# Performance work log

Measured on AMD Instinct MI355X. Metric: run time of the kernel, lower is better.

## Reference

```python
import jax, jax.numpy as jnp
import numpy as np

N, F, K, FP = 4096, 256, 8, 64  # nodes, in-feat, heads, out-feat per head
NEG_SLOPE = 0.2
MASK_FILL = -1e30  # stand-in for -inf (numerically safe under softmax/vjp)


def setup_inputs() -> dict:
    key = jax.random.key(0)
    k1, k2, k3, k4, k5 = jax.random.split(key, 5)
    x = jax.random.normal(k1, (N, F), dtype=jnp.float32)
    mask = jax.random.randint(k2, (1, N, N), 0, 2).astype(bool)
    idx = jnp.arange(N)
    mask = mask.at[0, idx, idx].set(True)  # self-loops guarantee no empty softmax rows
    W_w = jax.random.normal(k3, (K * FP, F), dtype=jnp.float32) * (1.0 / np.sqrt(F))
    W_b = jnp.zeros((K * FP,), dtype=jnp.float32)
    a_left = jax.random.normal(k4, (1, K, FP), dtype=jnp.float32) * 0.1
    a_right = jax.random.normal(k5, (1, K, FP), dtype=jnp.float32) * 0.1
    return {"x": x, "W_w": W_w, "W_b": W_b, "a_left": a_left, "a_right": a_right, "mask": mask}


def reference(x, W_w, W_b, a_left, a_right, mask):
    k, fp = a_left.shape[1], a_left.shape[2]
    # W(x): (N, K*F') -> (N, K, F')   [dropout p=0.0 -> identity]
    xe = (x @ W_w.T + W_b).reshape(-1, k, fp)
    # additive scores: h_left (K,N,1) + h_right (K,1,N) -> e (K,N,N)
    hl = jnp.einsum('nkf,kf->kn', xe, a_left[0])
    hr = jnp.einsum('nkf,kf->kn', xe, a_right[0])
    e = hl[:, :, None] + hr[:, None, :]
    e = jnp.where(e > 0, e, NEG_SLOPE * e)          # LeakyReLU(0.2)
    e = jnp.where(mask, e, MASK_FILL)               # masked_fill(~mask, -inf)
    a = jax.nn.softmax(e, axis=-1)                  # (K,N,N)
    # weighted sum of neighbor features: (K,N,N) x (N,K,F') -> (N,K,F')
    h_prime = jnp.einsum('knm,mkf->nkf', a, xe)
    h_prime = jax.nn.elu(h_prime)
    # non-final layer: elu again (as in source) then concat heads
    out = jax.nn.elu(h_prime).reshape(-1, k * fp)   # (N, K*F')
    return (out, mask)
```

## Files before the change

### kernel.cpp

```cpp
#include <hip/hip_runtime.h>
#include <hip/hip_bf16.h>

#define N_NODES 4096
#define F_IN    256
#define KH      8
#define KF      512
#define NEG_SLOPE 0.2f
#define EBIAS   4.0f

typedef _Float16 half8v __attribute__((ext_vector_type(8)));
typedef _Float16 half2v __attribute__((ext_vector_type(2)));
typedef __attribute__((ext_vector_type(4))) float floatx4;

union H8U4 { half8v v; unsigned u[4]; };

__device__ __forceinline__ unsigned short f2h(float f) {
    _Float16 h = (_Float16)f;
    unsigned short u; __builtin_memcpy(&u, &h, 2);
    return u;
}
__device__ __forceinline__ half2v asH2(unsigned u) {
    half2v h; __builtin_memcpy(&h, &u, 4);
    return h;
}
__device__ __forceinline__ unsigned asU(half2v h) {
    unsigned u; __builtin_memcpy(&u, &h, 4);
    return u;
}

__global__ __launch_bounds__(256) void mask_fused(
    const int* __restrict__ mask, float* __restrict__ outm,
    unsigned long long* __restrict__ bits) {
  const int tid = threadIdx.x;
  const size_t t4 = (size_t)blockIdx.x * 256 + tid;
  const int4 mv = ((const int4*)mask)[t4];
  float4 o;
  o.x = mv.x ? 1.f : 0.f; o.y = mv.y ? 1.f : 0.f;
  o.z = mv.z ? 1.f : 0.f; o.w = mv.w ? 1.f : 0.f;
  ((float4*)outm)[t4] = o;
  const unsigned nib = (mv.x ? 1u : 0u) | (mv.y ? 2u : 0u) |
                       (mv.z ? 4u : 0u) | (mv.w ? 8u : 0u);
  unsigned long long wv = (unsigned long long)nib << (4 * (tid & 15));
  wv |= __shfl_xor(wv, 1);
  wv |= __shfl_xor(wv, 2);
  wv |= __shfl_xor(wv, 4);
  wv |= __shfl_xor(wv, 8);
  if ((tid & 15) == 0) {
    const size_t e0 = t4 << 2;
    const size_t n = e0 >> 12;
    const size_t c = (e0 & 4095) >> 6;
    bits[c * N_NODES + n] = wv;
  }
}

__global__ __launch_bounds__(256) void mask_pack(
    const int* __restrict__ mask, unsigned long long* __restrict__ bits) {
  const size_t idx = (size_t)blockIdx.x * 256 + threadIdx.x;
  const unsigned long long b = __ballot(mask[idx] != 0);
  if ((threadIdx.x & 63) == 0) {
    const size_t w = idx >> 6;
    bits[(w & 63) * (size_t)N_NODES + (w >> 6)] = b;
  }
}
__global__ __launch_bounds__(256) void mask_copy(
    const int* __restrict__ mask, float* __restrict__ outm) {
  const size_t i4 = (size_t)blockIdx.x * 256 + threadIdx.x;
  const int4 mv = ((const int4*)mask)[i4];
  float4 o;
  o.x = mv.x ? 1.f : 0.f; o.y = mv.y ? 1.f : 0.f;
  o.z = mv.z ? 1.f : 0.f; o.w = mv.w ? 1.f : 0.f;
  ((float4*)outm)[i4] = o;
}

__global__ __launch_bounds__(256) void xe_gemm(
    const float* __restrict__ x,
    const float* __restrict__ Ww,
    const float* __restrict__ Wb,
    const float* __restrict__ al,
    const float* __restrict__ ar,
    unsigned short* __restrict__ xeB,
    float* __restrict__ hl,
    unsigned* __restrict__ EA,
    unsigned* __restrict__ EB,
    float* __restrict__ bmax) {
  __shared__ float As[32][65];
  __shared__ float Bs[32][65];
  __shared__ float redmax[4];
  const int tid = threadIdx.x;
  const int n0 = blockIdx.x * 64;
  const int j0 = blockIdx.y * 64;
  const int lr = tid >> 2;
  const int lc = (tid & 3) * 8;
  const int ty = tid >> 4;
  const int tx = tid & 15;
  float c[4][4];
  #pragma unroll
  for (int i = 0; i < 4; ++i)
    #pragma unroll
    for (int j = 0; j < 4; ++j) c[i][j] = 0.f;

  for (int f0 = 0; f0 < F_IN; f0 += 32) {
    const float* ap = x  + (size_t)(n0 + lr) * F_IN + f0 + lc;
    const float* bp = Ww + (size_t)(j0 + lr) * F_IN + f0 + lc;
    const float4 a0 = *(const float4*)ap;
    const float4 a1 = *(const float4*)(ap + 4);
    const float4 b0 = *(const float4*)bp;
    const float4 b1 = *(const float4*)(bp + 4);
    __syncthreads();
    As[lc + 0][lr] = a0.x; As[lc + 1][lr] = a0.y;
    As[lc + 2][lr] = a0.z; As[lc + 3][lr] = a0.w;
    As[lc + 4][lr] = a1.x; As[lc + 5][lr] = a1.y;
    As[lc + 6][lr] = a1.z; As[lc + 7][lr] = a1.w;
    Bs[lc + 0][lr] = b0.x; Bs[lc + 1][lr] = b0.y;
    Bs[lc + 2][lr] = b0.z; Bs[lc + 3][lr] = b0.w;
    Bs[lc + 4][lr] = b1.x; Bs[lc + 5][lr] = b1.y;
    Bs[lc + 6][lr] = b1.z; Bs[lc + 7][lr] = b1.w;
    __syncthreads();
    #pragma unroll
    for (int kk = 0; kk < 32; ++kk) {
      const float4 av = *(const float4*)&As[kk][ty * 4];
      const float4 bv = *(const float4*)&Bs[kk][tx * 4];
      const float a4[4] = {av.x, av.y, av.z, av.w};
      const float b4[4] = {bv.x, bv.y, bv.z, bv.w};
      #pragma unroll
      for (int i = 0; i < 4; ++i)
        #pragma unroll
        for (int j = 0; j < 4; ++j) c[i][j] = fmaf(a4[i], b4[j], c[i][j]);
    }
  }
  const float4 wb4 = *(const float4*)(Wb + j0 + tx * 4);
  const float4 al4 = *(const float4*)(al + j0 + tx * 4);
  const float4 ar4 = *(const float4*)(ar + j0 + tx * 4);
  const float wb[4] = {wb4.x, wb4.y, wb4.z, wb4.w};
  const float alv[4] = {al4.x, al4.y, al4.z, al4.w};
  const float arv[4] = {ar4.x, ar4.y, ar4.z, ar4.w};
  float v[4][4];
  float pl[4], pr[4];
  #pragma unroll
  for (int i = 0; i < 4; ++i) {
    float sl = 0.f, sr = 0.f;
    #pragma unroll
    for (int j = 0; j < 4; ++j) {
      v[i][j] = c[i][j] + wb[j];
      sl = fmaf(v[i][j], alv[j], sl);
      sr = fmaf(v[i][j], arv[j], sr);
    }
    pl[i] = sl; pr[i] = sr;
  }
  {
    const int k   = blockIdx.y;
    const int ft  = tx >> 2;
    const int fb  = (tx & 3) * 4;
    const int cc  = blockIdx.x;
    const int h_  = ty >> 3;
    const int qd  = (ty >> 1) & 3;
    const int jj0 = (ty & 1) * 4;
    unsigned short* tile = xeB + ((((size_t)(k * 4 + ft)) * 64 + cc) << 10)
                         + h_ * 512 + qd * 8 + jj0;
    #pragma unroll
    for (int j = 0; j < 4; ++j) {
      ushort4 pk;
      pk.x = f2h(v[0][j]); pk.y = f2h(v[1][j]);
      pk.z = f2h(v[2][j]); pk.w = f2h(v[3][j]);
      *(ushort4*)(tile + (fb + j) * 32) = pk;
    }
  }
  #pragma unroll
  for (int off = 8; off > 0; off >>= 1) {
    #pragma unroll
    for (int i = 0; i < 4; ++i) {
      pl[i] += __shfl_down(pl[i], off);
      pr[i] += __shfl_down(pr[i], off);
    }
  }
  if (tx == 0) {
    const int k = blockIdx.y;
    float4 o0 = {pl[0], pl[1], pl[2], pl[3]};
    *(float4*)(hl + k * N_NODES + n0 + ty * 4) = o0;
    unsigned short e1[4], e2[4];
    #pragma unroll
    for (int i = 0; i < 4; ++i) {
      e1[i] = f2h(__expf(pr[i] - EBIAS));
      e2[i] = f2h(__expf(NEG_SLOPE * (pr[i] - EBIAS)));
    }
    uint2 wa, wbv;
    wa.x  = (unsigned)e1[0] | ((unsigned)e1[1] << 16);
    wa.y  = (unsigned)e1[2] | ((unsigned)e1[3] << 16);
    wbv.x = (unsigned)e2[0] | ((unsigned)e2[1] << 16);
    wbv.y = (unsigned)e2[2] | ((unsigned)e2[3] << 16);
    *(uint2*)(EA + k * 2048 + ((n0 + ty * 4) >> 1)) = wa;
    *(uint2*)(EB + k * 2048 + ((n0 + ty * 4) >> 1)) = wbv;
  }
  float bm = (tx == 0)
      ? fmaxf(fmaxf(pr[0], pr[1]), fmaxf(pr[2], pr[3])) : -1e30f;
  bm = fmaxf(bm, __shfl_xor(bm, 16));
  bm = fmaxf(bm, __shfl_xor(bm, 32));
  if ((tid & 63) == 0) redmax[tid >> 6] = bm;
  __syncthreads();
  if (tid == 0) {
    bmax[blockIdx.y * 64 + blockIdx.x] =
        fmaxf(fmaxf(redmax[0], redmax[1]), fmaxf(redmax[2], redmax[3]));
  }
}

__global__ __launch_bounds__(256, 2) void gat_attn(
    const unsigned long long* __restrict__ mbitsT,
    const float* __restrict__ hl,
    const float* __restrict__ bmax,
    const unsigned* __restrict__ EA,
    const unsigned* __restrict__ EB,
    const unsigned short* __restrict__ xeB,
    float* __restrict__ out) {
  __shared__ float lds_acc[4][64][20];
  const int t = threadIdx.x;
  const int w4 = t >> 6;
  const int lane = t & 63;
  const int k  = blockIdx.x & 7;
  const int rg = blockIdx.x >> 3;
  const int n0 = rg * 32;
  const int row = lane & 15;
  const int quad = lane >> 4;
  const int q8 = quad * 8;

  float hm = bmax[k * 64 + lane];
  #pragma unroll
  for (int o = 1; o < 64; o <<= 1) hm = fmaxf(hm, __shfl_xor(hm, o));

  const float* hlp = hl + k * N_NODES + n0 + row;
  const float hlA = hlp[0];
  const float hlB = hlp[16];
  const float sA = hlA + hm;
  const float MA = fmaxf(sA, NEG_SLOPE * sA);
  const float sB = hlB + hm;
  const float MB = fmaxf(sB, NEG_SLOPE * sB);
  const float c1Af = __expf(hlA + EBIAS - MA);
  const float c2Af = __expf(NEG_SLOPE * (hlA + EBIAS) - MA);
  const float c1Bf = __expf(hlB + EBIAS - MB);
  const float c2Bf = __expf(NEG_SLOPE * (hlB + EBIAS) - MB);
  const half2v c1A = {(_Float16)c1Af, (_Float16)c1Af};
  const half2v c2A = {(_Float16)c2Af, (_Float16)c2Af};
  const half2v c1B = {(_Float16)c1Bf, (_Float16)c1Bf};
  const half2v c2B = {(_Float16)c2Bf, (_Float16)c2Bf};

  const int c0 = w4 * 16;
  const int cEnd = c0 + 16;

  const unsigned* pEA = EA + k * 2048 + c0 * 32 + quad * 4;
  const unsigned* pEB = EB + k * 2048 + c0 * 32 + quad * 4;
  const unsigned long long* pM = mbitsT + (size_t)c0 * N_NODES + n0 + row;
  const unsigned short* pB = xeB + (((size_t)k * 4) << 16)
                           + ((size_t)c0 << 10) + row * 32 + q8;

  half8v ones;
  #pragma unroll
  for (int i = 0; i < 8; ++i) ones[i] = (_Float16)1.0f;

  floatx4 accA[4], accB[4];
  #pragma unroll
  for (int ft = 0; ft < 4; ++ft) {
    accA[ft] = (floatx4){0.f, 0.f, 0.f, 0.f};
    accB[ft] = (floatx4){0.f, 0.f, 0.f, 0.f};
  }
  floatx4 dpA = (floatx4){0.f, 0.f, 0.f, 0.f};
  floatx4 dpB = (floatx4){0.f, 0.f, 0.f, 0.f};

  uint4 pA0 = *(const uint4*)pEA;
  uint4 pA1 = *(const uint4*)(pEA + 16);
  uint4 pB0 = *(const uint4*)pEB;
  uint4 pB1 = *(const uint4*)(pEB + 16);
  unsigned long long pMvA = pM[0];
  unsigned long long pMvB = pM[16];

  for (int cc = c0; cc < cEnd; ++cc) {
    half8v b0, b1, b2, b3, b4, b5, b6, b7;
    b0 = *(const half8v*)pB;                     b1 = *(const half8v*)(pB + 512);
    b2 = *(const half8v*)(pB + (64 << 10));      b3 = *(const half8v*)(pB + (64 << 10) + 512);
    b4 = *(const half8v*)(pB + (128 << 10));     b5 = *(const half8v*)(pB + (128 << 10) + 512);
    b6 = *(const half8v*)(pB + (192 << 10));     b7 = *(const half8v*)(pB + (192 << 10) + 512);
    pB += 1024;
    const uint4 eA0 = pA0, eA1 = pA1, eB0 = pB0, eB1 = pB1;
    const unsigned long long mbA = pMvA, mbB = pMvB;
    pEA += 32; pEB += 32; pM += N_NODES;
    if (cc + 1 < cEnd) {
      pA0 = *(const uint4*)pEA;
      pA1 = *(const uint4*)(pEA + 16);
      pB0 = *(const uint4*)pEB;
      pB1 = *(const uint4*)(pEB + 16);
      pMvA = pM[0];
      pMvB = pM[16];
    }
    const unsigned ea_lo[4] = {eA0.x, eA0.y, eA0.z, eA0.w};
    const unsigned eb_lo[4] = {eB0.x, eB0.y, eB0.z, eB0.w};
    const unsigned ea_hi[4] = {eA1.x, eA1.y, eA1.z, eA1.w};
    const unsigned eb_hi[4] = {eB1.x, eB1.y, eB1.z, eB1.w};
    {
      const unsigned mlo = (unsigned)(mbA >> q8);
      const unsigned mhi = (unsigned)(mbA >> (32 + q8));
      H8U4 a0, a1;
      #pragma unroll
      for (int p = 0; p < 4; ++p) {
        const half2v w2 = __builtin_elementwise_max(c1A * asH2(ea_lo[p]),
                                                    c2A * asH2(eb_lo[p]));
        const unsigned tb = mlo >> (2 * p);
        a0.u[p] = asU(w2) & (((tb & 1u) | ((tb & 2u) << 15)) * 0xFFFFu);
      }
      #pragma unroll
      for (int p = 0; p < 4; ++p) {
        const half2v w2 = __builtin_elementwise_max(c1A * asH2(ea_hi[p]),
                                                    c2A * asH2(eb_hi[p]));
        const unsigned tb = mhi >> (2 * p);
        a1.u[p] = asU(w2) & (((tb & 1u) | ((tb & 2u) << 15)) * 0xFFFFu);
      }
      dpA = __builtin_amdgcn_mfma_f32_16x16x32_f16(a0.v, ones, dpA, 0, 0, 0);
      dpA = __builtin_amdgcn_mfma_f32_16x16x32_f16(a1.v, ones, dpA, 0, 0, 0);
      accA[0] = __builtin_amdgcn_mfma_f32_16x16x32_f16(a0.v, b0, accA[0], 0, 0, 0);
      accA[0] = __builtin_amdgcn_mfma_f32_16x16x32_f16(a1.v, b1, accA[0], 0, 0, 0);
      accA[1] = __builtin_amdgcn_mfma_f32_16x16x32_f16(a0.v, b2, accA[1], 0, 0, 0);
      accA[1] = __builtin_amdgcn_mfma_f32_16x16x32_f16(a1.v, b3, accA[1], 0, 0, 0);
      accA[2] = __builtin_amdgcn_mfma_f32_16x16x32_f16(a0.v, b4, accA[2], 0, 0, 0);
      accA[2] = __builtin_amdgcn_mfma_f32_16x16x32_f16(a1.v, b5, accA[2], 0, 0, 0);
      accA[3] = __builtin_amdgcn_mfma_f32_16x16x32_f16(a0.v, b6, accA[3], 0, 0, 0);
      accA[3] = __builtin_amdgcn_mfma_f32_16x16x32_f16(a1.v, b7, accA[3], 0, 0, 0);
    }
    {
      const unsigned mlo = (unsigned)(mbB >> q8);
      const unsigned mhi = (unsigned)(mbB >> (32 + q8));
      H8U4 a0, a1;
      #pragma unroll
      for (int p = 0; p < 4; ++p) {
        const half2v w2 = __builtin_elementwise_max(c1B * asH2(ea_lo[p]),
                                                    c2B * asH2(eb_lo[p]));
        const unsigned tb = mlo >> (2 * p);
        a0.u[p] = asU(w2) & (((tb & 1u) | ((tb & 2u) << 15)) * 0xFFFFu);
      }
      #pragma unroll
      for (int p = 0; p < 4; ++p) {
        const half2v w2 = __builtin_elementwise_max(c1B * asH2(ea_hi[p]),
                                                    c2B * asH2(eb_hi[p]));
        const unsigned tb = mhi >> (2 * p);
        a1.u[p] = asU(w2) & (((tb & 1u) | ((tb & 2u) << 15)) * 0xFFFFu);
      }
      dpB = __builtin_amdgcn_mfma_f32_16x16x32_f16(a0.v, ones, dpB, 0, 0, 0);
      dpB = __builtin_amdgcn_mfma_f32_16x16x32_f16(a1.v, ones, dpB, 0, 0, 0);
      accB[0] = __builtin_amdgcn_mfma_f32_16x16x32_f16(a0.v, b0, accB[0], 0, 0, 0);
      accB[0] = __builtin_amdgcn_mfma_f32_16x16x32_f16(a1.v, b1, accB[0], 0, 0, 0);
      accB[1] = __builtin_amdgcn_mfma_f32_16x16x32_f16(a0.v, b2, accB[1], 0, 0, 0);
      accB[1] = __builtin_amdgcn_mfma_f32_16x16x32_f16(a1.v, b3, accB[1], 0, 0, 0);
      accB[2] = __builtin_amdgcn_mfma_f32_16x16x32_f16(a0.v, b4, accB[2], 0, 0, 0);
      accB[2] = __builtin_amdgcn_mfma_f32_16x16x32_f16(a1.v, b5, accB[2], 0, 0, 0);
      accB[3] = __builtin_amdgcn_mfma_f32_16x16x32_f16(a0.v, b6, accB[3], 0, 0, 0);
      accB[3] = __builtin_amdgcn_mfma_f32_16x16x32_f16(a1.v, b7, accB[3], 0, 0, 0);
    }
  }

  #pragma unroll
  for (int i = 0; i < 16; ++i) lds_acc[w4][lane][i] = accA[i >> 2][i & 3];
  #pragma unroll
  for (int i = 0; i < 4; ++i) lds_acc[w4][lane][16 + i] = dpA[i];
  __syncthreads();
  #pragma unroll
  for (int j = 0; j < 4; ++j) {
    const int sl = 4 * w4 + j;
    float fa = 0.f, dpt = 0.f;
    #pragma unroll
    for (int w2 = 0; w2 < 4; ++w2) {
      fa  += lds_acc[w2][lane][sl];
      dpt += lds_acc[w2][lane][16 + j];
    }
    float v = fa / dpt;
    v = (v > 0.f) ? v : (__expf(v) - 1.f);
    v = (v > 0.f) ? v : (__expf(v) - 1.f);
    out[(size_t)(n0 + quad * 4 + j) * KF + k * 64 + w4 * 16 + row] = v;
  }
  __syncthreads();
  #pragma unroll
  for (int i = 0; i < 16; ++i) lds_acc[w4][lane][i] = accB[i >> 2][i & 3];
  #pragma unroll
  for (int i = 0; i < 4; ++i) lds_acc[w4][lane][16 + i] = dpB[i];
  __syncthreads();
  #pragma unroll
  for (int j = 0; j < 4; ++j) {
    const int sl = 4 * w4 + j;
    float fa = 0.f, dpt = 0.f;
    #pragma unroll
    for (int w2 = 0; w2 < 4; ++w2) {
      fa  += lds_acc[w2][lane][sl];
      dpt += lds_acc[w2][lane][16 + j];
    }
    float v = fa / dpt;
    v = (v > 0.f) ? v : (__expf(v) - 1.f);
    v = (v > 0.f) ? v : (__expf(v) - 1.f);
    out[(size_t)(n0 + 16 + quad * 4 + j) * KF + k * 64 + w4 * 16 + row] = v;
  }
}

extern "C" void kernel_launch(void* const* d_in, const int* in_sizes, int n_in,
                              void* d_out, int out_size, void* d_ws, size_t ws_size,
                              hipStream_t stream) {
  const float* x    = (const float*)d_in[0];
  const float* Ww   = (const float*)d_in[1];
  const float* Wb   = (const float*)d_in[2];
  const float* al   = (const float*)d_in[3];
  const float* ar   = (const float*)d_in[4];
  const int*   mask = (const int*)d_in[5];

  float* out      = (float*)d_out;
  float* out_mask = out + (size_t)N_NODES * KF;

  const bool use_ws = (ws_size >= (8u << 20));
  char* scratch = use_ws ? (char*)d_ws : (char*)out_mask;
  unsigned short* xeB  = (unsigned short*)scratch;
  float*          hl   = (float*)(scratch + (4u << 20));
  unsigned*       EA   = (unsigned*)(hl + KH * N_NODES);
  unsigned*       EB   = EA + KH * 2048;
  float*          bmax = (float*)(EB + KH * 2048);
  unsigned long long* mbitsT = (unsigned long long*)(scratch + (5u << 20));

  dim3 ga(N_NODES / 64, KF / 64);
  xe_gemm<<<ga, 256, 0, stream>>>(x, Ww, Wb, al, ar, xeB, hl, EA, EB, bmax);

  if (use_ws) {
    mask_fused<<<(N_NODES * (size_t)N_NODES) / 1024, 256, 0, stream>>>(
        mask, out_mask, mbitsT);
    gat_attn<<<128 * KH, 256, 0, stream>>>(mbitsT, hl, bmax, EA, EB, xeB, out);
  } else {
    mask_pack<<<(N_NODES * (size_t)N_NODES) / 256, 256, 0, stream>>>(mask, mbitsT);
    gat_attn<<<128 * KH, 256, 0, stream>>>(mbitsT, hl, bmax, EA, EB, xeB, out);
    mask_copy<<<(N_NODES * (size_t)N_NODES) / (4 * 256), 256, 0, stream>>>(mask, out_mask);
  }
}
```

Measured before the change: 203.7 us.

## Rewrite xe projection GEMM with fp16 MFMA and per-wave max reduction

Replaces the LDS-tiled fp32 FMA GEMM for the feature projection with a register-direct fp16 MFMA 16x16x32 kernel. Each wave computes 16 rows times 64 columns, loading operands straight from global memory and converting them to half. The per-block max moves to per-wave outputs, and the attention kernel now reduces them with a float4 load, which removes the LDS reduction and barrier. This lowers the cost of the small GEMM stage but rounds the GEMM inputs to fp16, which reduces precision, and the loads are not staged through LDS.

```diff
diff --git a/kernel.cpp b/kernel.cpp
--- a/kernel.cpp
+++ b/kernel.cpp
@@ -26,6 +26,16 @@
 __device__ __forceinline__ unsigned asU(half2v h) {
     unsigned u; __builtin_memcpy(&u, &h, 4);
     return u;
+}
+__device__ __forceinline__ half8v ld8f(const float* p) {
+    const float4 a = *(const float4*)p;
+    const float4 b = *(const float4*)(p + 4);
+    half8v h;
+    h[0] = (_Float16)a.x; h[1] = (_Float16)a.y;
+    h[2] = (_Float16)a.z; h[3] = (_Float16)a.w;
+    h[4] = (_Float16)b.x; h[5] = (_Float16)b.y;
+    h[6] = (_Float16)b.z; h[7] = (_Float16)b.w;
+    return h;
 }
 
 __global__ __launch_bounds__(256) void mask_fused(
@@ -83,124 +93,86 @@
     unsigned* __restrict__ EA,
     unsigned* __restrict__ EB,
     float* __restrict__ bmax) {
-  __shared__ float As[32][65];
-  __shared__ float Bs[32][65];
-  __shared__ float redmax[4];
   const int tid = threadIdx.x;
-  const int n0 = blockIdx.x * 64;
-  const int j0 = blockIdx.y * 64;
-  const int lr = tid >> 2;
-  const int lc = (tid & 3) * 8;
-  const int ty = tid >> 4;
-  const int tx = tid & 15;
-  float c[4][4];
-  #pragma unroll
-  for (int i = 0; i < 4; ++i)
-    #pragma unroll
-    for (int j = 0; j < 4; ++j) c[i][j] = 0.f;
-
-  for (int f0 = 0; f0 < F_IN; f0 += 32) {
-    const float* ap = x  + (size_t)(n0 + lr) * F_IN + f0 + lc;
-    const float* bp = Ww + (size_t)(j0 + lr) * F_IN + f0 + lc;
-    const float4 a0 = *(const float4*)ap;
-    const float4 a1 = *(const float4*)(ap + 4);
-    const float4 b0 = *(const float4*)bp;
-    const float4 b1 = *(const float4*)(bp + 4);
-    __syncthreads();
-    As[lc + 0][lr] = a0.x; As[lc + 1][lr] = a0.y;
-    As[lc + 2][lr] = a0.z; As[lc + 3][lr] = a0.w;
-    As[lc + 4][lr] = a1.x; As[lc + 5][lr] = a1.y;
-    As[lc + 6][lr] = a1.z; As[lc + 7][lr] = a1.w;
-    Bs[lc + 0][lr] = b0.x; Bs[lc + 1][lr] = b0.y;
-    Bs[lc + 2][lr] = b0.z; Bs[lc + 3][lr] = b0.w;
-    Bs[lc + 4][lr] = b1.x; Bs[lc + 5][lr] = b1.y;
-    Bs[lc + 6][lr] = b1.z; Bs[lc + 7][lr] = b1.w;
-    __syncthreads();
-    #pragma unroll
-    for (int kk = 0; kk < 32; ++kk) {
-      const float4 av = *(const float4*)&As[kk][ty * 4];
-      const float4 bv = *(const float4*)&Bs[kk][tx * 4];
-      const float a4[4] = {av.x, av.y, av.z, av.w};
-      const float b4[4] = {bv.x, bv.y, bv.z, bv.w};
-      #pragma unroll
-      for (int i = 0; i < 4; ++i)
-        #pragma unroll
-        for (int j = 0; j < 4; ++j) c[i][j] = fmaf(a4[i], b4[j], c[i][j]);
-    }
-  }
-  const float4 wb4 = *(const float4*)(Wb + j0 + tx * 4);
-  const float4 al4 = *(const float4*)(al + j0 + tx * 4);
-  const float4 ar4 = *(const float4*)(ar + j0 + tx * 4);
-  const float wb[4] = {wb4.x, wb4.y, wb4.z, wb4.w};
-  const float alv[4] = {al4.x, al4.y, al4.z, al4.w};
-  const float arv[4] = {ar4.x, ar4.y, ar4.z, ar4.w};
-  float v[4][4];
-  float pl[4], pr[4];
-  #pragma unroll
-  for (int i = 0; i < 4; ++i) {
-    float sl = 0.f, sr = 0.f;
-    #pragma unroll
-    for (int j = 0; j < 4; ++j) {
-      v[i][j] = c[i][j] + wb[j];
-      sl = fmaf(v[i][j], alv[j], sl);
-      sr = fmaf(v[i][j], arv[j], sr);
-    }
-    pl[i] = sl; pr[i] = sr;
-  }
-  {
-    const int k   = blockIdx.y;
-    const int ft  = tx >> 2;
-    const int fb  = (tx & 3) * 4;
-    const int cc  = blockIdx.x;
-    const int h_  = ty >> 3;
-    const int qd  = (ty >> 1) & 3;
-    const int jj0 = (ty & 1) * 4;
-    unsigned short* tile = xeB + ((((size_t)(k * 4 + ft)) * 64 + cc) << 10)
-                         + h_ * 512 + qd * 8 + jj0;
-    #pragma unroll
-    for (int j = 0; j < 4; ++j) {
-      ushort4 pk;
-      pk.x = f2h(v[0][j]); pk.y = f2h(v[1][j]);
-      pk.z = f2h(v[2][j]); pk.w = f2h(v[3][j]);
-      *(ushort4*)(tile + (fb + j) * 32) = pk;
-    }
-  }
-  #pragma unroll
-  for (int off = 8; off > 0; off >>= 1) {
+  const int w = tid >> 6;
+  const int lane = tid & 63;
+  const int col16 = lane & 15;
+  const int quad = lane >> 4;
+  const int bx = blockIdx.x;
+  const int k  = blockIdx.y;
+  const int n0 = bx * 64;
+
+  const int rowA = n0 + w * 16 + col16;
+  const float* xp  = x  + (size_t)rowA * F_IN + quad * 8;
+  const float* wwp = Ww + (size_t)(k * 64 + col16) * F_IN + quad * 8;
+
+  floatx4 acc[4];
+  #pragma unroll
+  for (int ft = 0; ft < 4; ++ft) acc[ft] = (floatx4){0.f, 0.f, 0.f, 0.f};
+
+  #pragma unroll
+  for (int ks = 0; ks < 8; ++ks) {
+    const half8v aF = ld8f(xp + ks * 32);
+    #pragma unroll
+    for (int ft = 0; ft < 4; ++ft) {
+      const half8v bF = ld8f(wwp + (size_t)(ft * 16) * F_IN + ks * 32);
+      acc[ft] = __builtin_amdgcn_mfma_f32_16x16x32_f16(aF, bF, acc[ft], 0, 0, 0);
+    }
+  }
+
+  float pl[4] = {0.f, 0.f, 0.f, 0.f};
+  float pr[4] = {0.f, 0.f, 0.f, 0.f};
+  const int xoff = (w >> 1) * 512 + col16 * 32
+                 + ((w & 1) * 2 + (quad >> 1)) * 8 + (quad & 1) * 4;
+  #pragma unroll
+  for (int ft = 0; ft < 4; ++ft) {
+    const int c = k * 64 + ft * 16 + col16;
+    const float wbv = Wb[c];
+    const float a_l = al[c];
+    const float a_r = ar[c];
+    float v[4];
+    ushort4 pk;
     #pragma unroll
     for (int i = 0; i < 4; ++i) {
-      pl[i] += __shfl_down(pl[i], off);
-      pr[i] += __shfl_down(pr[i], off);
-    }
-  }
-  if (tx == 0) {
-    const int k = blockIdx.y;
+      v[i] = acc[ft][i] + wbv;
+      pl[i] = fmaf(v[i], a_l, pl[i]);
+      pr[i] = fmaf(v[i], a_r, pr[i]);
+    }
+    pk.x = f2h(v[0]); pk.y = f2h(v[1]); pk.z = f2h(v[2]); pk.w = f2h(v[3]);
+    unsigned short* tile = xeB + ((((size_t)(k * 4 + ft)) * 64 + bx) << 10);
+    *(ushort4*)(tile + xoff) = pk;
+  }
+  #pragma unroll
+  for (int o = 8; o > 0; o >>= 1) {
+    #pragma unroll
+    for (int i = 0; i < 4; ++i) {
+      pl[i] += __shfl_xor(pl[i], o);
+      pr[i] += __shfl_xor(pr[i], o);
+    }
+  }
+  if (col16 == 0) {
+    const int n = n0 + w * 16 + quad * 4;
     float4 o0 = {pl[0], pl[1], pl[2], pl[3]};
-    *(float4*)(hl + k * N_NODES + n0 + ty * 4) = o0;
+    *(float4*)(hl + k * N_NODES + n) = o0;
     unsigned short e1[4], e2[4];
     #pragma unroll
     for (int i = 0; i < 4; ++i) {
       e1[i] = f2h(__expf(pr[i] - EBIAS));
       e2[i] = f2h(__expf(NEG_SLOPE * (pr[i] - EBIAS)));
     }
-    uint2 wa, wbv;
-    wa.x  = (unsigned)e1[0] | ((unsigned)e1[1] << 16);
-    wa.y  = (unsigned)e1[2] | ((unsigned)e1[3] << 16);
-    wbv.x = (unsigned)e2[0] | ((unsigned)e2[1] << 16);
-    wbv.y = (unsigned)e2[2] | ((unsigned)e2[3] << 16);
-    *(uint2*)(EA + k * 2048 + ((n0 + ty * 4) >> 1)) = wa;
-    *(uint2*)(EB + k * 2048 + ((n0 + ty * 4) >> 1)) = wbv;
-  }
-  float bm = (tx == 0)
+    uint2 wa, wbv2;
+    wa.x   = (unsigned)e1[0] | ((unsigned)e1[1] << 16);
+    wa.y   = (unsigned)e1[2] | ((unsigned)e1[3] << 16);
+    wbv2.x = (unsigned)e2[0] | ((unsigned)e2[1] << 16);
+    wbv2.y = (unsigned)e2[2] | ((unsigned)e2[3] << 16);
+    *(uint2*)(EA + k * 2048 + (n >> 1)) = wa;
+    *(uint2*)(EB + k * 2048 + (n >> 1)) = wbv2;
+  }
+  float bm = (col16 == 0)
       ? fmaxf(fmaxf(pr[0], pr[1]), fmaxf(pr[2], pr[3])) : -1e30f;
   bm = fmaxf(bm, __shfl_xor(bm, 16));
   bm = fmaxf(bm, __shfl_xor(bm, 32));
-  if ((tid & 63) == 0) redmax[tid >> 6] = bm;
-  __syncthreads();
-  if (tid == 0) {
-    bmax[blockIdx.y * 64 + blockIdx.x] =
-        fmaxf(fmaxf(redmax[0], redmax[1]), fmaxf(redmax[2], redmax[3]));
-  }
+  if (lane == 0) bmax[k * 256 + bx * 4 + w] = bm;
 }
 
 __global__ __launch_bounds__(256, 2) void gat_attn(
@@ -222,7 +194,8 @@
   const int quad = lane >> 4;
   const int q8 = quad * 8;
 
-  float hm = bmax[k * 64 + lane];
+  const float4 bm4 = ((const float4*)bmax)[k * 64 + lane];
+  float hm = fmaxf(fmaxf(bm4.x, bm4.y), fmaxf(bm4.z, bm4.w));
   #pragma unroll
   for (int o = 1; o < 64; o <<= 1) hm = fmaxf(hm, __shfl_xor(hm, o));
 
@@ -416,7 +389,7 @@
   float*          bmax = (float*)(EB + KH * 2048);
   unsigned long long* mbitsT = (unsigned long long*)(scratch + (5u << 20));
 
-  dim3 ga(N_NODES / 64, KF / 64);
+  dim3 ga(N_NODES / 64, KH);
   xe_gemm<<<ga, 256, 0, stream>>>(x, Ww, Wb, al, ar, xeB, hl, EA, EB, bmax);
 
   if (use_ws) {
```

Result: no change. 201.8 us (-0.9%).
